# Performance work log

Measured on AMD Instinct MI355X. Metric: run time of the kernel, lower is better.

The kernel has to match this reference:

```python
import jax, jax.numpy as jnp
import numpy as np

N = 50000      # nodes
E = 800000     # edges (before self loops)
IN = 128       # in_ch
HID = 128      # hid (conv1 concat output)
OUT = 128      # out_ch
H = 4          # heads in conv1
NEG_SLOPE = 0.2


def setup_inputs() -> dict:
    key = jax.random.key(0)
    ks = jax.random.split(key, 16)
    s = 0.05
    return {
        "x": jax.random.normal(ks[0], (N, IN), dtype=jnp.float32),
        "edge_index": jax.random.randint(ks[1], (2, E), 0, N, dtype=jnp.int64),
        # conv1 params (heads=4, per-head dim HID//H)
        "W1l": jax.random.normal(ks[2], (IN, HID), dtype=jnp.float32) * s,
        "b1l": jnp.zeros((HID,), jnp.float32),
        "W1r": jax.random.normal(ks[3], (IN, HID), dtype=jnp.float32) * s,
        "b1r": jnp.zeros((HID,), jnp.float32),
        "att1": jax.random.normal(ks[4], (H, HID // H), dtype=jnp.float32) * s,
        "bias1": jnp.zeros((HID,), jnp.float32),
        # conv2 params (heads=1)
        "W2l": jax.random.normal(ks[5], (HID, OUT), dtype=jnp.float32) * s,
        "b2l": jnp.zeros((OUT,), jnp.float32),
        "W2r": jax.random.normal(ks[6], (HID, OUT), dtype=jnp.float32) * s,
        "b2r": jnp.zeros((OUT,), jnp.float32),
        "att2": jax.random.normal(ks[7], (1, OUT), dtype=jnp.float32) * s,
        "bias2": jnp.zeros((OUT,), jnp.float32),
    }


def gatv2_conv(x, src, dst, Wl, bl, Wr, br, att, heads):
    """PyG GATv2Conv (share_weights=False, concat=True).
    message(j->i): e = LeakyReLU(x_l[j] + x_r[i]); logit = <e, att>;
    softmax over edges per destination i; out_i = sum alpha * x_l[j].
    """
    n = x.shape[0]
    c = Wl.shape[1] // heads
    xl = (x @ Wl + bl).reshape(n, heads, c)   # source transform
    xr = (x @ Wr + br).reshape(n, heads, c)   # destination transform
    e = jax.nn.leaky_relu(xl[src] + xr[dst], NEG_SLOPE)      # [E, H, C]
    logits = jnp.einsum("ehc,hc->eh", e, att)                 # [E, H]
    m = jax.lax.stop_gradient(
        jax.ops.segment_max(logits, dst, num_segments=n))     # [N, H]
    p = jnp.exp(logits - m[dst])                              # [E, H]
    denom = jax.ops.segment_sum(p, dst, num_segments=n)       # [N, H]
    alpha = p / denom[dst]                                    # [E, H]
    out = jax.ops.segment_sum(xl[src] * alpha[..., None], dst,
                              num_segments=n)                 # [N, H, C]
    return out.reshape(n, heads * c)


def reference(x, edge_index, W1l, b1l, W1r, b1r, att1, bias1,
              W2l, b2l, W2r, b2r, att2, bias2):
    n = x.shape[0]
    # PyG default add_self_loops=True
    loops = jnp.arange(n, dtype=edge_index.dtype)
    src = jnp.concatenate([edge_index[0], loops])
    dst = jnp.concatenate([edge_index[1], loops])
    h = gatv2_conv(x, src, dst, W1l, b1l, W1r, b1r, att1, H) + bias1
    h = jax.nn.relu(h)
    out = gatv2_conv(h, src, dst, W2l, b2l, W2r, b2r, att2, 1) + bias2
    return out
```

## Files before the change

### kernel.cpp

```cpp
#include <hip/hip_runtime.h>
#include <hip/hip_bf16.h>

#define NODES 50000
#define NEDGE 800000
#define CH 128
#define NEG_SLOPE 0.2f
#define SCAN_CHUNK 2048
#define NBLK ((NODES + SCAN_CHUNK - 1) / SCAN_CHUNK)
#define NINF -1.0e30f
#define LOG2E 1.44269504088896340736f
#define NSLICE 400
#define SSLICE (NEDGE / NSLICE)
#define ZB ((NODES + 255) / 256)

typedef short short8 __attribute__((ext_vector_type(8)));
typedef float f32x4 __attribute__((ext_vector_type(4)));

__device__ __forceinline__ unsigned fbits(float f) {
    union { float f; unsigned u; } v; v.f = f; return v.u;
}
__device__ __forceinline__ float asf(unsigned u) {
    union { float f; unsigned u; } v; v.u = u; return v.f;
}
__device__ __forceinline__ unsigned short f2bf(float f) {
    unsigned u = fbits(f);
    unsigned r = u + 0x7fff + ((u >> 16) & 1);
    return (unsigned short)(r >> 16);
}
__device__ __forceinline__ float bf2f(unsigned short h) {
    return asf(((unsigned)h) << 16);
}
__device__ __forceinline__ float lrelu(float x) {
    return fmaxf(x, NEG_SLOPE * x);
}
__device__ __forceinline__ void bf8cvt(uint4 u, float* f) {
    f[0] = asf(u.x << 16); f[1] = asf(u.x & 0xFFFF0000u);
    f[2] = asf(u.y << 16); f[3] = asf(u.y & 0xFFFF0000u);
    f[4] = asf(u.z << 16); f[5] = asf(u.z & 0xFFFF0000u);
    f[6] = asf(u.w << 16); f[7] = asf(u.w & 0xFFFF0000u);
}
__device__ __forceinline__ int dset(int dst) {
    return (int)(((unsigned)dst * 8u) / 50000u);
}

__global__ __launch_bounds__(256) void prep_kernel(const void* idx, int* flag,
                                                   int* cnt,
                                                   const float* __restrict__ W0,
                                                   const float* __restrict__ W1,
                                                   const float* __restrict__ W2,
                                                   const float* __restrict__ W3,
                                                   unsigned short* __restrict__ wbase) {
    int b = (int)blockIdx.x;
    if (b < ZB) {
        int t = b * 256 + (int)threadIdx.x;
        if (t < NODES) cnt[t] = 0;
        if (b == 0 && threadIdx.x < 64) {
            const int* w = (const int*)idx;
            int nz = (w[2 * threadIdx.x + 1] != 0) ? 1 : 0;
            unsigned long long bal = __ballot(nz);
            if (threadIdx.x == 0) *flag = (bal == 0ull) ? 1 : 0;
        }
        return;
    }
    int wb = b - ZB;
    int which = wb >> 6;
    const float* W = (which == 0) ? W0 : (which == 1) ? W1 : (which == 2) ? W2 : W3;
    unsigned short* hiT = wbase + (size_t)which * 32768;
    unsigned short* loT = hiT + 16384;
    int i = (wb & 63) * 256 + (int)threadIdx.x;
    int k = i >> 7, n = i & 127;
    float f = W[i];
    unsigned short h = f2bf(f);
    unsigned short l = f2bf(f - bf2f(h));
    hiT[n * CH + k] = h;
    loT[n * CH + k] = l;
}

__global__ __launch_bounds__(256) void hist_part_kernel(const void* idx,
                                                        const int* flag,
                                                        int* cnt) {
    int set = blockIdx.x & 7;
    int slice = blockIdx.x >> 3;
    int base = slice * SSLICE;
    int endE = base + SSLICE;
    int i64 = *flag;
    const int* w = (const int*)idx;
    for (int e = base + (int)threadIdx.x; e < endE; e += 256) {
        int dst = i64 ? w[2 * (NEDGE + e)] : w[NEDGE + e];
        if (dset(dst) == set) atomicAdd(&cnt[dst], 1);
    }
}

__global__ __launch_bounds__(256) void scan1_kernel(const int* __restrict__ cnt,
                                                    int* __restrict__ bsum) {
    int base = blockIdx.x * SCAN_CHUNK + (int)threadIdx.x * 8;
    int s = 0;
    #pragma unroll
    for (int k = 0; k < 8; ++k) {
        int i = base + k;
        s += (i < NODES) ? cnt[i] : 0;
    }
    #pragma unroll
    for (int m = 1; m < 64; m <<= 1) s += __shfl_xor(s, m);
    __shared__ int ws[4];
    if ((threadIdx.x & 63) == 0) ws[threadIdx.x >> 6] = s;
    __syncthreads();
    if (threadIdx.x == 0) bsum[blockIdx.x] = ws[0] + ws[1] + ws[2] + ws[3];
}

__global__ __launch_bounds__(256) void scan3_kernel(const int* __restrict__ cnt,
                                                    const int* __restrict__ bsum,
                                                    int* __restrict__ offs,
                                                    int* __restrict__ cursor) {
    int tid = (int)threadIdx.x;
    int bpre = 0;
    #pragma unroll
    for (int b = 0; b < NBLK; ++b) bpre += (b < (int)blockIdx.x) ? bsum[b] : 0;

    int base = blockIdx.x * SCAN_CHUNK + tid * 8;
    int v[8];
    int s = 0;
    #pragma unroll
    for (int k = 0; k < 8; ++k) {
        int i = base + k;
        v[k] = (i < NODES) ? cnt[i] : 0;
        s += v[k];
    }
    int lane = tid & 63;
    int incl = s;
    #pragma unroll
    for (int m = 1; m < 64; m <<= 1) {
        int t = __shfl_up(incl, m);
        if (lane >= m) incl += t;
    }
    __shared__ int wtot[4];
    if (lane == 63) wtot[tid >> 6] = incl;
    __syncthreads();
    int w = tid >> 6;
    int wbase = 0;
    #pragma unroll
    for (int k = 0; k < 4; ++k) wbase += (k < w) ? wtot[k] : 0;
    int excl = bpre + wbase + (incl - s);
    #pragma unroll
    for (int k = 0; k < 8; ++k) {
        int i = base + k;
        if (i < NODES) { offs[i] = excl; cursor[i] = excl; }
        excl += v[k];
    }
    if (blockIdx.x == 0 && tid == 0) offs[NODES] = NEDGE;
}

__global__ __launch_bounds__(256) void scatter_part_kernel(const void* idx,
                                                           const int* flag,
                                                           int* cursor,
                                                           int* __restrict__ srcs) {
    int set = blockIdx.x & 7;
    int slice = blockIdx.x >> 3;
    int base = slice * SSLICE;
    int endE = base + SSLICE;
    int i64 = *flag;
    const int* w = (const int*)idx;
    for (int e = base + (int)threadIdx.x; e < endE; e += 256) {
        int dst = i64 ? w[2 * (NEDGE + e)] : w[NEDGE + e];
        if (dset(dst) == set) {
            int src = i64 ? w[2 * e] : w[e];
            int pos = atomicAdd(&cursor[dst], 1);
            srcs[pos] = src;
        }
    }
}

#define GR 64
#define LDP 136

__global__ __launch_bounds__(256) void gemm_dual_mfma(
        const float* __restrict__ X,
        const unsigned short* __restrict__ whTl, const unsigned short* __restrict__ wlTl,
        const unsigned short* __restrict__ whTr, const unsigned short* __restrict__ wlTr,
        const float* __restrict__ bl, const float* __restrict__ br,
        unsigned short* __restrict__ Ylb, float* __restrict__ Yr, int nrows) {
    __shared__ unsigned short xh[GR][LDP];
    __shared__ unsigned short xlo[GR][LDP];

    int r0 = blockIdx.x * GR;
    int tid = (int)threadIdx.x;

    {
        int row = tid >> 2;
        int c0 = (tid & 3) * 32;
        const float* src = X + (size_t)(r0 + row) * CH + c0;
        bool valid = (r0 + row) < nrows;
        #pragma unroll
        for (int j = 0; j < 32; j += 4) {
            float4 v = valid ? *(const float4*)(src + j)
                             : make_float4(0.f, 0.f, 0.f, 0.f);
            unsigned ux = fbits(v.x), uy = fbits(v.y);
            unsigned uz = fbits(v.z), uw = fbits(v.w);
            unsigned hx = ux & 0xFFFF0000u, hy = uy & 0xFFFF0000u;
            unsigned hz = uz & 0xFFFF0000u, hw = uw & 0xFFFF0000u;
            uint2 hp;
            hp.x = (ux >> 16) | hy;
            hp.y = (uz >> 16) | hw;
            float lx = v.x - asf(hx), ly = v.y - asf(hy);
            float lz = v.z - asf(hz), lw = v.w - asf(hw);
            uint2 lp;
            lp.x = (fbits(lx) >> 16) | (fbits(ly) & 0xFFFF0000u);
            lp.y = (fbits(lz) >> 16) | (fbits(lw) & 0xFFFF0000u);
            *(uint2*)&xh[row][c0 + j]  = hp;
            *(uint2*)&xlo[row][c0 + j] = lp;
        }
    }
    __syncthreads();

    int wave = tid >> 6;
    int lane = tid & 63;
    int l15 = lane & 15, q = lane >> 4;

    f32x4 acc[4][4];
    #pragma unroll
    for (int mt = 0; mt < 4; ++mt)
        #pragma unroll
        for (int nt = 0; nt < 4; ++nt) acc[mt][nt] = (f32x4)0.f;

    const unsigned short* bhp[4];
    const unsigned short* blp_[4];
    int ncol[4];
    #pragma unroll
    for (int nt = 0; nt < 4; ++nt) {
        int n = (wave * 4 + nt) * 16 + l15;
        ncol[nt] = n;
        int nn = n & 127;
        bhp[nt]  = ((n < CH) ? whTl : whTr) + (size_t)nn * CH;
        blp_[nt] = ((n < CH) ? wlTl : wlTr) + (size_t)nn * CH;
    }

    for (int kt = 0; kt < 4; ++kt) {
        int kofs = kt * 32 + q * 8;
        short8 ah[4], al[4];
        #pragma unroll
        for (int mt = 0; mt < 4; ++mt) {
            ah[mt] = *(const short8*)&xh[mt * 16 + l15][kofs];
            al[mt] = *(const short8*)&xlo[mt * 16 + l15][kofs];
        }
        #pragma unroll
        for (int nt = 0; nt < 4; ++nt) {
            short8 bh8 = *(const short8*)(bhp[nt] + kofs);
            short8 bl8 = *(const short8*)(blp_[nt] + kofs);
            #pragma unroll
            for (int mt = 0; mt < 4; ++mt) {
                acc[mt][nt] = __builtin_amdgcn_mfma_f32_16x16x32_bf16(
                                  ah[mt], bh8, acc[mt][nt], 0, 0, 0);
                acc[mt][nt] = __builtin_amdgcn_mfma_f32_16x16x32_bf16(
                                  al[mt], bh8, acc[mt][nt], 0, 0, 0);
                acc[mt][nt] = __builtin_amdgcn_mfma_f32_16x16x32_bf16(
                                  ah[mt], bl8, acc[mt][nt], 0, 0, 0);
            }
        }
    }

    #pragma unroll
    for (int nt = 0; nt < 4; ++nt) {
        int n = ncol[nt];
        int nc = n & 127;
        if (n < CH) {
            float bv = bl[nc];
            #pragma unroll
            for (int mt = 0; mt < 4; ++mt)
                #pragma unroll
                for (int reg = 0; reg < 4; ++reg) {
                    int row = r0 + mt * 16 + q * 4 + reg;
                    if (row < nrows)
                        Ylb[(size_t)row * CH + nc] = f2bf(acc[mt][nt][reg] + bv);
                }
        } else {
            float bv = br[nc];
            #pragma unroll
            for (int mt = 0; mt < 4; ++mt)
                #pragma unroll
                for (int reg = 0; reg < 4; ++reg) {
                    int row = r0 + mt * 16 + q * 4 + reg;
                    if (row < nrows)
                        Yr[(size_t)row * CH + nc] = acc[mt][nt][reg] + bv;
                }
        }
    }
}

__global__ __launch_bounds__(256) void gemm_dual_mfma_pl(
        const unsigned short* __restrict__ Ah, const unsigned short* __restrict__ Al,
        const unsigned short* __restrict__ whTl, const unsigned short* __restrict__ wlTl,
        const unsigned short* __restrict__ whTr, const unsigned short* __restrict__ wlTr,
        const float* __restrict__ bl, const float* __restrict__ br,
        unsigned short* __restrict__ Ylb, float* __restrict__ Yr, int nrows) {
    int r0 = blockIdx.x * GR;
    int tid = (int)threadIdx.x;
    int wave = tid >> 6;
    int lane = tid & 63;
    int l15 = lane & 15, q = lane >> 4;

    size_t offA[4];
    #pragma unroll
    for (int mt = 0; mt < 4; ++mt) {
        int row = r0 + mt * 16 + l15;
        if (row > nrows - 1) row = nrows - 1;
        offA[mt] = (size_t)row * CH;
    }

    f32x4 acc[4][4];
    #pragma unroll
    for (int mt = 0; mt < 4; ++mt)
        #pragma unroll
        for (int nt = 0; nt < 4; ++nt) acc[mt][nt] = (f32x4)0.f;

    const unsigned short* bhp[4];
    const unsigned short* blp_[4];
    int ncol[4];
    #pragma unroll
    for (int nt = 0; nt < 4; ++nt) {
        int n = (wave * 4 + nt) * 16 + l15;
        ncol[nt] = n;
        int nn = n & 127;
        bhp[nt]  = ((n < CH) ? whTl : whTr) + (size_t)nn * CH;
        blp_[nt] = ((n < CH) ? wlTl : wlTr) + (size_t)nn * CH;
    }

    for (int kt = 0; kt < 4; ++kt) {
        int kofs = kt * 32 + q * 8;
        short8 ah[4], al[4];
        #pragma unroll
        for (int mt = 0; mt < 4; ++mt) {
            ah[mt] = *(const short8*)(Ah + offA[mt] + kofs);
            al[mt] = *(const short8*)(Al + offA[mt] + kofs);
        }
        #pragma unroll
        for (int nt = 0; nt < 4; ++nt) {
            short8 bh8 = *(const short8*)(bhp[nt] + kofs);
            short8 bl8 = *(const short8*)(blp_[nt] + kofs);
            #pragma unroll
            for (int mt = 0; mt < 4; ++mt) {
                acc[mt][nt] = __builtin_amdgcn_mfma_f32_16x16x32_bf16(
                                  ah[mt], bh8, acc[mt][nt], 0, 0, 0);
                acc[mt][nt] = __builtin_amdgcn_mfma_f32_16x16x32_bf16(
                                  al[mt], bh8, acc[mt][nt], 0, 0, 0);
                acc[mt][nt] = __builtin_amdgcn_mfma_f32_16x16x32_bf16(
                                  ah[mt], bl8, acc[mt][nt], 0, 0, 0);
            }
        }
    }

    #pragma unroll
    for (int nt = 0; nt < 4; ++nt) {
        int n = ncol[nt];
        int nc = n & 127;
        if (n < CH) {
            float bv = bl[nc];
            #pragma unroll
            for (int mt = 0; mt < 4; ++mt)
                #pragma unroll
                for (int reg = 0; reg < 4; ++reg) {
                    int row = r0 + mt * 16 + q * 4 + reg;
                    if (row < nrows)
                        Ylb[(size_t)row * CH + nc] = f2bf(acc[mt][nt][reg] + bv);
                }
        } else {
            float bv = br[nc];
            #pragma unroll
            for (int mt = 0; mt < 4; ++mt)
                #pragma unroll
                for (int reg = 0; reg < 4; ++reg) {
                    int row = r0 + mt * 16 + q * 4 + reg;
                    if (row < nrows)
                        Yr[(size_t)row * CH + nc] = acc[mt][nt][reg] + bv;
                }
        }
    }
}

template <int HEADS, bool RELU, bool SPLITOUT>
__global__ __launch_bounds__(256) void node_pass(
        const unsigned short* __restrict__ xlb,
        const float* __restrict__ xr,
        const float* __restrict__ att,
        const float* __restrict__ bias,
        const int* __restrict__ offs, const int* __restrict__ srcs,
        float* __restrict__ outf,
        unsigned short* __restrict__ outh, unsigned short* __restrict__ outl) {
    constexpr int GL = (CH / HEADS) / 8;
    int wave = (int)threadIdx.x >> 6;
    int i = blockIdx.x * 4 + wave;
    int lane = (int)threadIdx.x & 63;
    int g = lane >> 4;
    int l16 = lane & 15;
    int c0 = l16 * 8;

    float r[8], a[8], s[8];
    {
        const float4* xrp = (const float4*)(xr + (size_t)i * CH + c0);
        float4 r0 = xrp[0], r1 = xrp[1];
        r[0]=r0.x; r[1]=r0.y; r[2]=r0.z; r[3]=r0.w;
        r[4]=r1.x; r[5]=r1.y; r[6]=r1.z; r[7]=r1.w;
        const float4* atp = (const float4*)(att + c0);
        float4 a0 = atp[0], a1 = atp[1];
        a[0]=a0.x*LOG2E; a[1]=a0.y*LOG2E; a[2]=a0.z*LOG2E; a[3]=a0.w*LOG2E;
        a[4]=a1.x*LOG2E; a[5]=a1.y*LOG2E; a[6]=a1.z*LOG2E; a[7]=a1.w*LOG2E;
    }
    uint4 us = *(const uint4*)(xlb + (size_t)i * CH + c0);
    bf8cvt(us, s);

    float ts = 0.f;
    #pragma unroll
    for (int c = 0; c < 8; ++c) ts += lrelu(s[c] + r[c]) * a[c];
    #pragma unroll
    for (int msk = 1; msk < GL; msk <<= 1) ts += __shfl_xor(ts, msk);

    float m = (g == 0) ? ts : NINF;
    float d = (g == 0) ? 1.f : 0.f;
    float acc[8];
    #pragma unroll
    for (int c = 0; c < 8; ++c) acc[c] = (g == 0) ? s[c] : 0.f;

    int beg = offs[i], end = offs[i + 1];
    int deg = end - beg;
    int iters = (deg + 7) >> 3;
    if (iters > 0) {
        int last = end - 1;
        int e = beg + g;
        int s0i = srcs[min(e, last)];
        int s1i = srcs[min(e + 4, last)];
        uint4 u0 = *(const uint4*)(xlb + (size_t)s0i * CH + c0);
        uint4 u1 = *(const uint4*)(xlb + (size_t)s1i * CH + c0);

        for (int it = 0; it < iters; ++it, e += 8) {
            bool v0 = e < end, v1 = (e + 4) < end;
            int sn0 = srcs[min(e + 8, last)];
            int sn1 = srcs[min(e + 12, last)];
            uint4 un0 = *(const uint4*)(xlb + (size_t)sn0 * CH + c0);
            uint4 un1 = *(const uint4*)(xlb + (size_t)sn1 * CH + c0);

            float f0[8], f1[8];
            bf8cvt(u0, f0);
            bf8cvt(u1, f1);
            float t0 = 0.f, t1 = 0.f;
            #pragma unroll
            for (int c = 0; c < 8; ++c) {
                t0 += lrelu(f0[c] + r[c]) * a[c];
                t1 += lrelu(f1[c] + r[c]) * a[c];
            }
            #pragma unroll
            for (int msk = 1; msk < GL; msk <<= 1) {
                t0 += __shfl_xor(t0, msk);
                t1 += __shfl_xor(t1, msk);
            }
            t0 = v0 ? t0 : NINF;
            t1 = v1 ? t1 : NINF;

            float nm = fmaxf(m, fmaxf(t0, t1));
            float sc = exp2f(m - nm);
            float p0 = v0 ? exp2f(t0 - nm) : 0.f;
            float p1 = v1 ? exp2f(t1 - nm) : 0.f;
            d = d * sc + p0 + p1;
            #pragma unroll
            for (int c = 0; c < 8; ++c)
                acc[c] = acc[c] * sc + p0 * f0[c] + p1 * f1[c];
            m = nm;
            u0 = un0; u1 = un1;
        }
    }

    #pragma unroll
    for (int msk = 16; msk <= 32; msk <<= 1) {
        float mo  = __shfl_xor(m, msk);
        float dof = __shfl_xor(d, msk);
        float nm = fmaxf(m, mo);
        float s0 = exp2f(m - nm), s1 = exp2f(mo - nm);
        d = d * s0 + dof * s1;
        #pragma unroll
        for (int c = 0; c < 8; ++c) {
            float ao = __shfl_xor(acc[c], msk);
            acc[c] = acc[c] * s0 + ao * s1;
        }
        m = nm;
    }

    if (g == 0) {
        float inv = 1.0f / d;
        const float4* bp = (const float4*)(bias + c0);
        float4 b0 = bp[0], b1 = bp[1];
        float bb[8] = {b0.x, b0.y, b0.z, b0.w, b1.x, b1.y, b1.z, b1.w};
        float o[8];
        #pragma unroll
        for (int c = 0; c < 8; ++c) {
            o[c] = acc[c] * inv + bb[c];
            if (RELU) o[c] = fmaxf(o[c], 0.f);
        }
        if (SPLITOUT) {
            unsigned hu[8];
            float lo[8];
            #pragma unroll
            for (int c = 0; c < 8; ++c) {
                hu[c] = fbits(o[c]) & 0xFFFF0000u;
                lo[c] = o[c] - asf(hu[c]);
            }
            uint4 ph, pl;
            ph.x = (hu[0] >> 16) | hu[1];  ph.y = (hu[2] >> 16) | hu[3];
            ph.z = (hu[4] >> 16) | hu[5];  ph.w = (hu[6] >> 16) | hu[7];
            pl.x = (fbits(lo[0]) >> 16) | (fbits(lo[1]) & 0xFFFF0000u);
            pl.y = (fbits(lo[2]) >> 16) | (fbits(lo[3]) & 0xFFFF0000u);
            pl.z = (fbits(lo[4]) >> 16) | (fbits(lo[5]) & 0xFFFF0000u);
            pl.w = (fbits(lo[6]) >> 16) | (fbits(lo[7]) & 0xFFFF0000u);
            *(uint4*)(outh + (size_t)i * CH + c0) = ph;
            *(uint4*)(outl + (size_t)i * CH + c0) = pl;
        } else {
            float4 w0 = make_float4(o[0], o[1], o[2], o[3]);
            float4 w1 = make_float4(o[4], o[5], o[6], o[7]);
            float4* op = (float4*)(outf + (size_t)i * CH + c0);
            op[0] = w0; op[1] = w1;
        }
    }
}

extern "C" void kernel_launch(void* const* d_in, const int* in_sizes, int n_in,
                              void* d_out, int out_size, void* d_ws, size_t ws_size,
                              hipStream_t stream) {
    const float* x     = (const float*)d_in[0];
    const void*  eidx  = d_in[1];
    const float* W1l   = (const float*)d_in[2];
    const float* b1l   = (const float*)d_in[3];
    const float* W1r   = (const float*)d_in[4];
    const float* b1r   = (const float*)d_in[5];
    const float* att1  = (const float*)d_in[6];
    const float* bias1 = (const float*)d_in[7];
    const float* W2l   = (const float*)d_in[8];
    const float* b2l   = (const float*)d_in[9];
    const float* W2r   = (const float*)d_in[10];
    const float* b2r   = (const float*)d_in[11];
    const float* att2  = (const float*)d_in[12];
    const float* bias2 = (const float*)d_in[13];
    float* out = (float*)d_out;

    unsigned short* xlb = (unsigned short*)d_ws;
    float* xr = (float*)(xlb + (size_t)NODES * CH);
    unsigned short* hbh = (unsigned short*)(xr + (size_t)NODES * CH);
    unsigned short* hbl = hbh + (size_t)NODES * CH;
    int* offs   = (int*)(hbl + (size_t)NODES * CH);
    int* cnt    = offs + (NODES + 1);
    int* cursor = cnt + NODES;
    int* srcs   = cursor + NODES;
    int* flag   = srcs + NEDGE;
    int* bsum   = flag + 1;
    unsigned short* wbuf =
        (unsigned short*)(((uintptr_t)(bsum + NBLK) + 15) & ~(uintptr_t)15);
    unsigned short* w1lh = wbuf;              unsigned short* w1ll = wbuf + 16384;
    unsigned short* w1rh = wbuf + 32768;      unsigned short* w1rl = wbuf + 49152;
    unsigned short* w2lh = wbuf + 65536;      unsigned short* w2ll = wbuf + 81920;
    unsigned short* w2rh = wbuf + 98304;      unsigned short* w2rl = wbuf + 114688;

    const int GG = (NODES + GR - 1) / GR;
    const int PG = NSLICE * 8;

    prep_kernel<<<ZB + 256, 256, 0, stream>>>(eidx, flag, cnt,
                                              W1l, W1r, W2l, W2r, wbuf);
    hist_part_kernel<<<PG, 256, 0, stream>>>(eidx, flag, cnt);
    scan1_kernel<<<NBLK, 256, 0, stream>>>(cnt, bsum);
    scan3_kernel<<<NBLK, 256, 0, stream>>>(cnt, bsum, offs, cursor);
    scatter_part_kernel<<<PG, 256, 0, stream>>>(eidx, flag, cursor, srcs);

    gemm_dual_mfma<<<GG, 256, 0, stream>>>(x, w1lh, w1ll, w1rh, w1rl,
                                           b1l, b1r, xlb, xr, NODES);
    node_pass<4, true, true><<<(NODES + 3) / 4, 256, 0, stream>>>(
        xlb, xr, att1, bias1, offs, srcs, nullptr, hbh, hbl);

    gemm_dual_mfma_pl<<<GG, 256, 0, stream>>>(hbh, hbl, w2lh, w2ll, w2rh, w2rl,
                                              b2l, b2r, xlb, xr, NODES);
    node_pass<1, false, false><<<(NODES + 3) / 4, 256, 0, stream>>>(
        xlb, xr, att2, bias2, offs, srcs, out, nullptr, nullptr);
}
```

Measured before the change: 376.3 us.

## Use packed f32x2 math and single-edge-per-group loop in node pass

Rewrites the node aggregation kernel to use two-wide float vectors so the compiler can emit packed FP32 instructions for the LeakyReLU, attention dot product and accumulator update. The inner loop now handles one edge per 16-lane group per iteration instead of two, prefetching one neighbor row ahead. This cuts VALU instruction count and register pressure, but halves memory-level parallelism per iteration and doubles the online-softmax serial steps.

```diff
diff --git a/kernel.cpp b/kernel.cpp
--- a/kernel.cpp
+++ b/kernel.cpp
@@ -15,6 +15,7 @@
 
 typedef short short8 __attribute__((ext_vector_type(8)));
 typedef float f32x4 __attribute__((ext_vector_type(4)));
+typedef float f32x2 __attribute__((ext_vector_type(2)));
 
 __device__ __forceinline__ unsigned fbits(float f) {
     union { float f; unsigned u; } v; v.f = f; return v.u;
@@ -30,14 +31,11 @@
 __device__ __forceinline__ float bf2f(unsigned short h) {
     return asf(((unsigned)h) << 16);
 }
-__device__ __forceinline__ float lrelu(float x) {
-    return fmaxf(x, NEG_SLOPE * x);
-}
-__device__ __forceinline__ void bf8cvt(uint4 u, float* f) {
-    f[0] = asf(u.x << 16); f[1] = asf(u.x & 0xFFFF0000u);
-    f[2] = asf(u.y << 16); f[3] = asf(u.y & 0xFFFF0000u);
-    f[4] = asf(u.z << 16); f[5] = asf(u.z & 0xFFFF0000u);
-    f[6] = asf(u.w << 16); f[7] = asf(u.w & 0xFFFF0000u);
+__device__ __forceinline__ void bf8cvt2(uint4 u, f32x2* f) {
+    f[0] = (f32x2){asf(u.x << 16), asf(u.x & 0xFFFF0000u)};
+    f[1] = (f32x2){asf(u.y << 16), asf(u.y & 0xFFFF0000u)};
+    f[2] = (f32x2){asf(u.z << 16), asf(u.z & 0xFFFF0000u)};
+    f[3] = (f32x2){asf(u.w << 16), asf(u.w & 0xFFFF0000u)};
 }
 __device__ __forceinline__ int dset(int dst) {
     return (int)(((unsigned)dst * 8u) / 50000u);
@@ -393,77 +391,73 @@
     int l16 = lane & 15;
     int c0 = l16 * 8;
 
-    float r[8], a[8], s[8];
+    f32x2 r2[4], a2[4], s2[4];
     {
         const float4* xrp = (const float4*)(xr + (size_t)i * CH + c0);
         float4 r0 = xrp[0], r1 = xrp[1];
-        r[0]=r0.x; r[1]=r0.y; r[2]=r0.z; r[3]=r0.w;
-        r[4]=r1.x; r[5]=r1.y; r[6]=r1.z; r[7]=r1.w;
+        r2[0] = (f32x2){r0.x, r0.y}; r2[1] = (f32x2){r0.z, r0.w};
+        r2[2] = (f32x2){r1.x, r1.y}; r2[3] = (f32x2){r1.z, r1.w};
         const float4* atp = (const float4*)(att + c0);
         float4 a0 = atp[0], a1 = atp[1];
-        a[0]=a0.x*LOG2E; a[1]=a0.y*LOG2E; a[2]=a0.z*LOG2E; a[3]=a0.w*LOG2E;
-        a[4]=a1.x*LOG2E; a[5]=a1.y*LOG2E; a[6]=a1.z*LOG2E; a[7]=a1.w*LOG2E;
+        a2[0] = (f32x2){a0.x, a0.y} * LOG2E; a2[1] = (f32x2){a0.z, a0.w} * LOG2E;
+        a2[2] = (f32x2){a1.x, a1.y} * LOG2E; a2[3] = (f32x2){a1.z, a1.w} * LOG2E;
     }
     uint4 us = *(const uint4*)(xlb + (size_t)i * CH + c0);
-    bf8cvt(us, s);
-
-    float ts = 0.f;
-    #pragma unroll
-    for (int c = 0; c < 8; ++c) ts += lrelu(s[c] + r[c]) * a[c];
+    bf8cvt2(us, s2);
+
+    f32x2 td = (f32x2)0.f;
+    #pragma unroll
+    for (int k = 0; k < 4; ++k) {
+        f32x2 z = s2[k] + r2[k];
+        f32x2 l = __builtin_elementwise_max(z, z * NEG_SLOPE);
+        td += l * a2[k];
+    }
+    float ts = td.x + td.y;
     #pragma unroll
     for (int msk = 1; msk < GL; msk <<= 1) ts += __shfl_xor(ts, msk);
 
     float m = (g == 0) ? ts : NINF;
     float d = (g == 0) ? 1.f : 0.f;
-    float acc[8];
-    #pragma unroll
-    for (int c = 0; c < 8; ++c) acc[c] = (g == 0) ? s[c] : 0.f;
+    f32x2 acc2[4];
+    #pragma unroll
+    for (int k = 0; k < 4; ++k) acc2[k] = (g == 0) ? s2[k] : (f32x2)0.f;
 
     int beg = offs[i], end = offs[i + 1];
     int deg = end - beg;
-    int iters = (deg + 7) >> 3;
+    int iters = (deg + 3) >> 2;
     if (iters > 0) {
         int last = end - 1;
         int e = beg + g;
-        int s0i = srcs[min(e, last)];
-        int s1i = srcs[min(e + 4, last)];
-        uint4 u0 = *(const uint4*)(xlb + (size_t)s0i * CH + c0);
-        uint4 u1 = *(const uint4*)(xlb + (size_t)s1i * CH + c0);
-
-        for (int it = 0; it < iters; ++it, e += 8) {
-            bool v0 = e < end, v1 = (e + 4) < end;
-            int sn0 = srcs[min(e + 8, last)];
-            int sn1 = srcs[min(e + 12, last)];
-            uint4 un0 = *(const uint4*)(xlb + (size_t)sn0 * CH + c0);
-            uint4 un1 = *(const uint4*)(xlb + (size_t)sn1 * CH + c0);
-
-            float f0[8], f1[8];
-            bf8cvt(u0, f0);
-            bf8cvt(u1, f1);
-            float t0 = 0.f, t1 = 0.f;
-            #pragma unroll
-            for (int c = 0; c < 8; ++c) {
-                t0 += lrelu(f0[c] + r[c]) * a[c];
-                t1 += lrelu(f1[c] + r[c]) * a[c];
+        int si = srcs[min(e, last)];
+        uint4 u = *(const uint4*)(xlb + (size_t)si * CH + c0);
+
+        for (int it = 0; it < iters; ++it, e += 4) {
+            bool valid = e < end;
+            int sn = srcs[min(e + 4, last)];
+            uint4 un = *(const uint4*)(xlb + (size_t)sn * CH + c0);
+
+            f32x2 f2[4];
+            bf8cvt2(u, f2);
+            f32x2 td2 = (f32x2)0.f;
+            #pragma unroll
+            for (int k = 0; k < 4; ++k) {
+                f32x2 z = f2[k] + r2[k];
+                f32x2 l = __builtin_elementwise_max(z, z * NEG_SLOPE);
+                td2 += l * a2[k];
             }
-            #pragma unroll
-            for (int msk = 1; msk < GL; msk <<= 1) {
-                t0 += __shfl_xor(t0, msk);
-                t1 += __shfl_xor(t1, msk);
-            }
-            t0 = v0 ? t0 : NINF;
-            t1 = v1 ? t1 : NINF;
-
-            float nm = fmaxf(m, fmaxf(t0, t1));
+            float t = td2.x + td2.y;
+            #pragma unroll
+            for (int msk = 1; msk < GL; msk <<= 1) t += __shfl_xor(t, msk);
+            t = valid ? t : NINF;
+
+            float nm = fmaxf(m, t);
             float sc = exp2f(m - nm);
-            float p0 = v0 ? exp2f(t0 - nm) : 0.f;
-            float p1 = v1 ? exp2f(t1 - nm) : 0.f;
-            d = d * sc + p0 + p1;
-            #pragma unroll
-            for (int c = 0; c < 8; ++c)
-                acc[c] = acc[c] * sc + p0 * f0[c] + p1 * f1[c];
+            float p  = valid ? exp2f(t - nm) : 0.f;
+            d = d * sc + p;
+            #pragma unroll
+            for (int k = 0; k < 4; ++k) acc2[k] = acc2[k] * sc + f2[k] * p;
             m = nm;
-            u0 = un0; u1 = un1;
+            u = un;
         }
     }
 
@@ -475,9 +469,11 @@
         float s0 = exp2f(m - nm), s1 = exp2f(mo - nm);
         d = d * s0 + dof * s1;
         #pragma unroll
-        for (int c = 0; c < 8; ++c) {
-            float ao = __shfl_xor(acc[c], msk);
-            acc[c] = acc[c] * s0 + ao * s1;
+        for (int k = 0; k < 4; ++k) {
+            f32x2 ao;
+            ao.x = __shfl_xor(acc2[k].x, msk);
+            ao.y = __shfl_xor(acc2[k].y, msk);
+            acc2[k] = acc2[k] * s0 + ao * s1;
         }
         m = nm;
     }
@@ -489,10 +485,13 @@
         float bb[8] = {b0.x, b0.y, b0.z, b0.w, b1.x, b1.y, b1.z, b1.w};
         float o[8];
         #pragma unroll
-        for (int c = 0; c < 8; ++c) {
-            o[c] = acc[c] * inv + bb[c];
+        for (int k = 0; k < 4; ++k) {
+            o[2*k]   = acc2[k].x * inv + bb[2*k];
+            o[2*k+1] = acc2[k].y * inv + bb[2*k+1];
+        }
+        #pragma unroll
+        for (int c = 0; c < 8; ++c)
             if (RELU) o[c] = fmaxf(o[c], 0.f);
-        }
         if (SPLITOUT) {
             unsigned hu[8];
             float lo[8];
```

New measurement: 364.2 us. 1.03x faster.
